# Performance work log

Measured on AMD Instinct MI355X. Metric: run time of the kernel, lower is better.

## Reference

```python
import jax, jax.numpy as jnp
import numpy as np

B, N, M = 16, 4096, 4096

def setup_inputs() -> dict:
    key = jax.random.key(0)
    k1, k2, k3 = jax.random.split(key, 3)
    src_points = jax.random.normal(k1, (B, N, 3), dtype=jnp.float32)
    tgt_points = jax.random.normal(k2, (B, M, 3), dtype=jnp.float32)
    weights = jax.random.uniform(k3, (B,), dtype=jnp.float32)
    return {"src_points": src_points, "tgt_points": tgt_points, "weights": weights}

def reference(src_points, tgt_points, weights):
    # Pairwise squared distances per batch: [B, N, M]
    # ||s - t||^2 = ||s||^2 + ||t||^2 - 2 s.t  (single dense intermediate)
    s2 = jnp.sum(src_points * src_points, axis=-1)  # [B, N]
    t2 = jnp.sum(tgt_points * tgt_points, axis=-1)  # [B, M]
    cross = jnp.einsum('bnd,bmd->bnm', src_points, tgt_points)  # [B, N, M]
    d2 = s2[:, :, None] + t2[:, None, :] - 2.0 * cross          # [B, N, M]
    d2 = jnp.maximum(d2, 0.0)  # numerical guard
    # Bidirectional chamfer: mean of nearest-neighbor squared distances
    d_src_to_tgt = jnp.mean(jnp.min(d2, axis=2), axis=1)  # [B]
    d_tgt_to_src = jnp.mean(jnp.min(d2, axis=1), axis=1)  # [B]
    distances = d_src_to_tgt + d_tgt_to_src               # [B]
    distances = distances * weights
    return jnp.mean(distances)  # reduction='mean'
```

## Files before the change

kernel.cpp:

```cpp
#include <hip/hip_runtime.h>

#define BQ 16
#define NP 4096
#define MP 4096

constexpr int TPB = 256;
constexpr int WAVES = 4;
constexpr int FR = 4;
constexpr int SRC_PER_BLOCK = 32 * FR * WAVES;
constexpr int TGT_PER_BLOCK = 1024;
constexpr int CHUNK = 256;

typedef __bf16 bf16x8 __attribute__((ext_vector_type(8)));
typedef float f32x16 __attribute__((ext_vector_type(16)));

union Frag {
    unsigned short u[8];
    bf16x8 v;
    int4 i4;
};

__device__ inline unsigned short f2bf(float f) {
    unsigned u = __float_as_uint(f);
    return (unsigned short)((u + 0x7FFFu + ((u >> 16) & 1u)) >> 16);
}
__device__ inline float bf2f(unsigned short h) {
    return __uint_as_float(((unsigned)h) << 16);
}

__global__ __launch_bounds__(TPB) void chamfer_prep_kernel(
    const float* __restrict__ srcp, const float* __restrict__ tgtp,
    unsigned short* __restrict__ table, unsigned int* __restrict__ minbuf,
    float* __restrict__ out) {
    const int idx = blockIdx.x * TPB + threadIdx.x;
    const int dir = idx >> 16;
    const int rem = idx & 65535;
    const float* rows = dir ? srcp : tgtp;
    const float* p = rows + (size_t)rem * 3;
    float x = p[0], y = p[1], z = p[2];
    unsigned short xh = f2bf(x), yh = f2bf(y), zh = f2bf(z);
    unsigned short xl = f2bf(x - bf2f(xh));
    unsigned short yl = f2bf(y - bf2f(yh));
    unsigned short zl = f2bf(z - bf2f(zh));
    float t2 = fmaf(x, x, fmaf(y, y, z * z));
    unsigned short t2h = f2bf(t2), t2l = f2bf(t2 - bf2f(t2h));
    const unsigned short ONE = 0x3F80;
    Frag p0, p1;
    p0.u[0] = xh; p0.u[1] = yh; p0.u[2] = zh;
    p0.u[3] = xh; p0.u[4] = yh; p0.u[5] = zh;
    p0.u[6] = xl; p0.u[7] = yl;
    p1.u[0] = zl;
    p1.u[1] = t2h; p1.u[2] = t2l;
    p1.u[3] = ONE; p1.u[4] = ONE;
    p1.u[5] = 0; p1.u[6] = 0; p1.u[7] = 0;
    int4* dst = (int4*)(table + (size_t)idx * 16);
    dst[0] = p0.i4;
    dst[1] = p1.i4;
    minbuf[idx] = 0x7F800000u;
    if (idx == 0) out[0] = 0.0f;
}

__global__ __launch_bounds__(TPB) void chamfer_main_kernel(
    const float* __restrict__ srcp, const float* __restrict__ tgtp,
    const unsigned short* __restrict__ table,
    unsigned int* __restrict__ minbuf) {
    const int gz  = blockIdx.z;
    const int dir = gz >> 4;
    const int b   = gz & 15;
    const float* S = dir ? (tgtp + (size_t)b * MP * 3) : (srcp + (size_t)b * NP * 3);
    const unsigned short* At =
        table + ((size_t)gz * 4096 + (size_t)blockIdx.y * TGT_PER_BLOCK) * 16;
    unsigned int* mb = minbuf + (size_t)gz * 4096;

    const int tid  = threadIdx.x;
    const int lane = tid & 63;
    const int half = lane >> 5;
    const int col  = lane & 31;
    const int wave = tid >> 6;

    __shared__ unsigned short sh[CHUNK * 16];
    const unsigned short ONE = 0x3F80;

    Frag bf[FR];
#pragma unroll
    for (int f = 0; f < FR; ++f) {
        const int sidx = blockIdx.x * SRC_PER_BLOCK + (wave * FR + f) * 32 + col;
        const float* sp = S + (size_t)sidx * 3;
        float x = sp[0], y = sp[1], z = sp[2];
        unsigned short uh0 = f2bf(-2.0f * x), uh1 = f2bf(-2.0f * y), uh2 = f2bf(-2.0f * z);
        unsigned short ul0 = f2bf(-2.0f * x - bf2f(uh0));
        unsigned short ul1 = f2bf(-2.0f * y - bf2f(uh1));
        unsigned short ul2 = f2bf(-2.0f * z - bf2f(uh2));
        float s2 = fmaf(x, x, fmaf(y, y, z * z));
        unsigned short s2h = f2bf(s2), s2l = f2bf(s2 - bf2f(s2h));
        if (half == 0) {
            bf[f].u[0] = uh0; bf[f].u[1] = uh1; bf[f].u[2] = uh2;
            bf[f].u[3] = ul0; bf[f].u[4] = ul1; bf[f].u[5] = ul2;
            bf[f].u[6] = uh0; bf[f].u[7] = uh1;
        } else {
            bf[f].u[0] = uh2; bf[f].u[1] = ONE; bf[f].u[2] = ONE;
            bf[f].u[3] = s2h; bf[f].u[4] = s2l;
            bf[f].u[5] = 0;   bf[f].u[6] = 0;  bf[f].u[7] = 0;
        }
    }

    float accm[FR];
#pragma unroll
    for (int f = 0; f < FR; ++f) accm[f] = __int_as_float(0x7F800000);

    const f32x16 zc = {};

    for (int c = 0; c < TGT_PER_BLOCK / CHUNK; ++c) {
        {
            const int4* gp = (const int4*)(At + (size_t)c * CHUNK * 16);
            int4* sp4 = (int4*)sh;
            sp4[tid]       = gp[tid];
            sp4[tid + 256] = gp[tid + 256];
        }
        __syncthreads();

#pragma unroll
        for (int sc = 0; sc < CHUNK / 32; ++sc) {
            Frag a;
            a.i4 = *(const int4*)&sh[sc * 512 + col * 16 + half * 8];
#pragma unroll
            for (int f = 0; f < FR; ++f) {
                f32x16 d = __builtin_amdgcn_mfma_f32_32x32x16_bf16(a.v, bf[f].v, zc, 0, 0, 0);
                float m0 = fminf(fminf(d[0], d[1]), d[2]);
                float m1 = fminf(fminf(d[3], d[4]), d[5]);
                float m2 = fminf(fminf(d[6], d[7]), d[8]);
                float m3 = fminf(fminf(d[9], d[10]), d[11]);
                float m4 = fminf(fminf(d[12], d[13]), d[14]);
                float t0 = fminf(fminf(m0, m1), m2);
                float t1 = fminf(fminf(m3, m4), d[15]);
                accm[f] = fminf(fminf(accm[f], t0), t1);
            }
        }
        __syncthreads();
    }

#pragma unroll
    for (int f = 0; f < FR; ++f) {
        float m = fminf(accm[f], __shfl_xor(accm[f], 32, 64));
        m = fmaxf(m, 0.0f);
        if (lane < 32) {
            const int sidx = blockIdx.x * SRC_PER_BLOCK + (wave * FR + f) * 32 + col;
            atomicMin(&mb[sidx], __float_as_uint(m));
        }
    }
}

__global__ __launch_bounds__(TPB) void chamfer_reduce_kernel(
    const float* __restrict__ minbuf, const float* __restrict__ weights,
    float* __restrict__ out) {
    const int idx = blockIdx.x;
    const int b = idx & 15;
    const float* m0 = minbuf + (size_t)idx * 4096;

    float s = 0.0f;
    for (int i = threadIdx.x; i < 4096; i += TPB) s += m0[i];
#pragma unroll
    for (int off = 32; off > 0; off >>= 1) s += __shfl_down(s, off, 64);

    __shared__ float red[TPB / 64];
    if ((threadIdx.x & 63) == 0) red[threadIdx.x >> 6] = s;
    __syncthreads();
    if (threadIdx.x == 0) {
        float tot = red[0] + red[1] + red[2] + red[3];
        atomicAdd(out, weights[b] * tot * (1.0f / (4096.0f * (float)BQ)));
    }
}

__global__ void chamfer_zero_kernel(float* __restrict__ out) { out[0] = 0.0f; }

__global__ __launch_bounds__(TPB) void chamfer_mfma_fb_kernel(
    const float* __restrict__ srcp, const float* __restrict__ tgtp,
    const float* __restrict__ wts, float* __restrict__ out) {
    const int gy = blockIdx.y, dir = gy >> 4, b = gy & 15;
    const float* S = dir ? (tgtp + (size_t)b * MP * 3) : (srcp + (size_t)b * NP * 3);
    const float* T = dir ? (srcp + (size_t)b * NP * 3) : (tgtp + (size_t)b * MP * 3);
    const int tid = threadIdx.x, lane = tid & 63, half = lane >> 5,
              col = tid & 31, wave = tid >> 6;
    __shared__ unsigned short sh[256 * 16];
    __shared__ float partial[4];
    const unsigned short ONE = 0x3F80;
    Frag bfrag;
    {
        const int sidx = blockIdx.x * 128 + wave * 32 + (lane & 31);
        const float* sp = S + (size_t)sidx * 3;
        float x = sp[0], y = sp[1], z = sp[2];
        unsigned short uh0 = f2bf(-2.0f * x), uh1 = f2bf(-2.0f * y), uh2 = f2bf(-2.0f * z);
        unsigned short ul0 = f2bf(-2.0f * x - bf2f(uh0));
        unsigned short ul1 = f2bf(-2.0f * y - bf2f(uh1));
        unsigned short ul2 = f2bf(-2.0f * z - bf2f(uh2));
        float s2 = fmaf(x, x, fmaf(y, y, z * z));
        unsigned short s2h = f2bf(s2), s2l = f2bf(s2 - bf2f(s2h));
        if (half == 0) {
            bfrag.u[0] = uh0; bfrag.u[1] = uh1; bfrag.u[2] = uh2;
            bfrag.u[3] = ul0; bfrag.u[4] = ul1; bfrag.u[5] = ul2;
            bfrag.u[6] = uh0; bfrag.u[7] = uh1;
        } else {
            bfrag.u[0] = uh2; bfrag.u[1] = ONE; bfrag.u[2] = ONE;
            bfrag.u[3] = s2h; bfrag.u[4] = s2l;
            bfrag.u[5] = 0;   bfrag.u[6] = 0;  bfrag.u[7] = 0;
        }
    }
    float accm = __int_as_float(0x7F800000);
    for (int c = 0; c < MP / 256; ++c) {
        {
            const float* tp = T + (size_t)(c * 256 + tid) * 3;
            float x = tp[0], y = tp[1], z = tp[2];
            unsigned short xh = f2bf(x), yh = f2bf(y), zh = f2bf(z);
            unsigned short xl = f2bf(x - bf2f(xh)), yl = f2bf(y - bf2f(yh)),
                           zl = f2bf(z - bf2f(zh));
            float t2 = fmaf(x, x, fmaf(y, y, z * z));
            unsigned short t2h = f2bf(t2), t2l = f2bf(t2 - bf2f(t2h));
            Frag p0, p1;
            p0.u[0] = xh; p0.u[1] = yh; p0.u[2] = zh;
            p0.u[3] = xh; p0.u[4] = yh; p0.u[5] = zh;
            p0.u[6] = xl; p0.u[7] = yl;
            p1.u[0] = zl; p1.u[1] = t2h; p1.u[2] = t2l;
            p1.u[3] = ONE; p1.u[4] = ONE; p1.u[5] = 0; p1.u[6] = 0; p1.u[7] = 0;
            const int sub = tid >> 5, row = tid & 31;
            *(int4*)&sh[sub * 512 + row * 8] = p0.i4;
            *(int4*)&sh[sub * 512 + 256 + row * 8] = p1.i4;
        }
        __syncthreads();
        const f32x16 zc = {};
#pragma unroll
        for (int sc = 0; sc < 8; ++sc) {
            Frag a;
            a.i4 = *(const int4*)&sh[sc * 512 + half * 256 + col * 8];
            f32x16 d = __builtin_amdgcn_mfma_f32_32x32x16_bf16(a.v, bfrag.v, zc, 0, 0, 0);
            float m0 = fminf(fminf(d[0], d[1]), d[2]);
            float m1 = fminf(fminf(d[3], d[4]), d[5]);
            float m2 = fminf(fminf(d[6], d[7]), d[8]);
            float m3 = fminf(fminf(d[9], d[10]), d[11]);
            float m4 = fminf(fminf(d[12], d[13]), d[14]);
            accm = fminf(accm, fminf(fminf(fminf(m0, m1), m2),
                                     fminf(fminf(m3, m4), d[15])));
        }
        __syncthreads();
    }
    float m = fminf(accm, __shfl_xor(accm, 32, 64));
    m = fmaxf(m, 0.0f);
#pragma unroll
    for (int off = 16; off > 0; off >>= 1) m += __shfl_xor(m, off, 64);
    if (lane == 0) partial[wave] = m;
    __syncthreads();
    if (tid == 0) {
        float v = partial[0] + partial[1] + partial[2] + partial[3];
        atomicAdd(out, v * wts[b] * (1.0f / ((float)NP * (float)BQ)));
    }
}

extern "C" void kernel_launch(void* const* d_in, const int* in_sizes, int n_in,
                              void* d_out, int out_size, void* d_ws, size_t ws_size,
                              hipStream_t stream) {
    const float* src = (const float*)d_in[0];
    const float* tgt = (const float*)d_in[1];
    const float* wts = (const float*)d_in[2];
    float* out = (float*)d_out;

    const size_t MINBUF_BYTES = (size_t)2 * BQ * 4096 * 4;
    const size_t TABLE_BYTES  = (size_t)2 * BQ * 4096 * 32;

    if (ws_size >= MINBUF_BYTES + TABLE_BYTES) {
        unsigned int* minbuf = (unsigned int*)d_ws;
        unsigned short* table = (unsigned short*)((char*)d_ws + MINBUF_BYTES);

        chamfer_prep_kernel<<<(2 * BQ * 4096) / TPB, TPB, 0, stream>>>(
            src, tgt, table, minbuf, out);

        dim3 grid(NP / SRC_PER_BLOCK, MP / TGT_PER_BLOCK, 2 * BQ);
        chamfer_main_kernel<<<grid, TPB, 0, stream>>>(src, tgt, table, minbuf);

        chamfer_reduce_kernel<<<2 * BQ, TPB, 0, stream>>>(
            (const float*)minbuf, wts, out);
    } else {
        chamfer_zero_kernel<<<1, 1, 0, stream>>>(out);
        dim3 grid(NP / 128, 2 * BQ);
        chamfer_mfma_fb_kernel<<<grid, TPB, 0, stream>>>(src, tgt, wts, out);
    }
}
```

Before: 93.37 us.

## Stream MFMA A-fragments directly from global table, dropping LDS staging and barriers

The main kernel no longer copies target chunks into shared memory with barriers. Each lane now loads its bf16 A-fragment straight from a prep-table layout reordered to match the MFMA fragment layout. The tiling also changes: two source fragments per wave instead of four and a target split of two, giving a different grid shape and fewer atomics per target. This removes LDS traffic and synchronisation but relies on global/L2 cache bandwidth, since four waves reread the same lines. The fallback kernel also gets a register-prefetch of the next chunk.

```diff
diff --git a/kernel.cpp b/kernel.cpp
--- a/kernel.cpp
+++ b/kernel.cpp
@@ -6,10 +6,10 @@
 
 constexpr int TPB = 256;
 constexpr int WAVES = 4;
-constexpr int FR = 4;
-constexpr int SRC_PER_BLOCK = 32 * FR * WAVES;
-constexpr int TGT_PER_BLOCK = 1024;
-constexpr int CHUNK = 256;
+constexpr int FR = 2;
+constexpr int COLS_PER_BLOCK = 32 * FR * WAVES;
+constexpr int ROWSPLIT = 2;
+constexpr int GROUPS_PER_BLOCK = (MP / 32) / ROWSPLIT;
 
 typedef __bf16 bf16x8 __attribute__((ext_vector_type(8)));
 typedef float f32x16 __attribute__((ext_vector_type(16)));
@@ -33,10 +33,12 @@
     unsigned short* __restrict__ table, unsigned int* __restrict__ minbuf,
     float* __restrict__ out) {
     const int idx = blockIdx.x * TPB + threadIdx.x;
-    const int dir = idx >> 16;
-    const int rem = idx & 65535;
-    const float* rows = dir ? srcp : tgtp;
-    const float* p = rows + (size_t)rem * 3;
+    const int gy  = idx >> 12;
+    const int t   = idx & 4095;
+    const int dir = gy >> 4, b = gy & 15;
+    const float* rows = dir ? (srcp + (size_t)b * NP * 3)
+                            : (tgtp + (size_t)b * MP * 3);
+    const float* p = rows + (size_t)t * 3;
     float x = p[0], y = p[1], z = p[2];
     unsigned short xh = f2bf(x), yh = f2bf(y), zh = f2bf(z);
     unsigned short xl = f2bf(x - bf2f(xh));
@@ -53,9 +55,9 @@
     p1.u[1] = t2h; p1.u[2] = t2l;
     p1.u[3] = ONE; p1.u[4] = ONE;
     p1.u[5] = 0; p1.u[6] = 0; p1.u[7] = 0;
-    int4* dst = (int4*)(table + (size_t)idx * 16);
-    dst[0] = p0.i4;
-    dst[1] = p1.i4;
+    unsigned short* dst = table + ((size_t)gy << 16) + ((t >> 5) << 9) + ((t & 31) << 4);
+    *(int4*)(dst)     = p0.i4;
+    *(int4*)(dst + 8) = p1.i4;
     minbuf[idx] = 0x7F800000u;
     if (idx == 0) out[0] = 0.0f;
 }
@@ -64,13 +66,11 @@
     const float* __restrict__ srcp, const float* __restrict__ tgtp,
     const unsigned short* __restrict__ table,
     unsigned int* __restrict__ minbuf) {
-    const int gz  = blockIdx.z;
-    const int dir = gz >> 4;
-    const int b   = gz & 15;
+    const int gy  = blockIdx.z;
+    const int dir = gy >> 4;
+    const int b   = gy & 15;
     const float* S = dir ? (tgtp + (size_t)b * MP * 3) : (srcp + (size_t)b * NP * 3);
-    const unsigned short* At =
-        table + ((size_t)gz * 4096 + (size_t)blockIdx.y * TGT_PER_BLOCK) * 16;
-    unsigned int* mb = minbuf + (size_t)gz * 4096;
+    unsigned int* mb = minbuf + ((size_t)gy << 12);
 
     const int tid  = threadIdx.x;
     const int lane = tid & 63;
@@ -78,13 +78,12 @@
     const int col  = lane & 31;
     const int wave = tid >> 6;
 
-    __shared__ unsigned short sh[CHUNK * 16];
     const unsigned short ONE = 0x3F80;
 
-    Frag bf[FR];
-#pragma unroll
-    for (int f = 0; f < FR; ++f) {
-        const int sidx = blockIdx.x * SRC_PER_BLOCK + (wave * FR + f) * 32 + col;
+    Frag bfr[FR];
+#pragma unroll
+    for (int f = 0; f < FR; ++f) {
+        const int sidx = blockIdx.x * COLS_PER_BLOCK + (wave * FR + f) * 32 + col;
         const float* sp = S + (size_t)sidx * 3;
         float x = sp[0], y = sp[1], z = sp[2];
         unsigned short uh0 = f2bf(-2.0f * x), uh1 = f2bf(-2.0f * y), uh2 = f2bf(-2.0f * z);
@@ -94,13 +93,13 @@
         float s2 = fmaf(x, x, fmaf(y, y, z * z));
         unsigned short s2h = f2bf(s2), s2l = f2bf(s2 - bf2f(s2h));
         if (half == 0) {
-            bf[f].u[0] = uh0; bf[f].u[1] = uh1; bf[f].u[2] = uh2;
-            bf[f].u[3] = ul0; bf[f].u[4] = ul1; bf[f].u[5] = ul2;
-            bf[f].u[6] = uh0; bf[f].u[7] = uh1;
+            bfr[f].u[0] = uh0; bfr[f].u[1] = uh1; bfr[f].u[2] = uh2;
+            bfr[f].u[3] = ul0; bfr[f].u[4] = ul1; bfr[f].u[5] = ul2;
+            bfr[f].u[6] = uh0; bfr[f].u[7] = uh1;
         } else {
-            bf[f].u[0] = uh2; bf[f].u[1] = ONE; bf[f].u[2] = ONE;
-            bf[f].u[3] = s2h; bf[f].u[4] = s2l;
-            bf[f].u[5] = 0;   bf[f].u[6] = 0;  bf[f].u[7] = 0;
+            bfr[f].u[0] = uh2; bfr[f].u[1] = ONE; bfr[f].u[2] = ONE;
+            bfr[f].u[3] = s2h; bfr[f].u[4] = s2l;
+            bfr[f].u[5] = 0;   bfr[f].u[6] = 0;  bfr[f].u[7] = 0;
         }
     }
 
@@ -110,33 +109,26 @@
 
     const f32x16 zc = {};
 
-    for (int c = 0; c < TGT_PER_BLOCK / CHUNK; ++c) {
-        {
-            const int4* gp = (const int4*)(At + (size_t)c * CHUNK * 16);
-            int4* sp4 = (int4*)sh;
-            sp4[tid]       = gp[tid];
-            sp4[tid + 256] = gp[tid + 256];
-        }
-        __syncthreads();
-
-#pragma unroll
-        for (int sc = 0; sc < CHUNK / 32; ++sc) {
-            Frag a;
-            a.i4 = *(const int4*)&sh[sc * 512 + col * 16 + half * 8];
-#pragma unroll
-            for (int f = 0; f < FR; ++f) {
-                f32x16 d = __builtin_amdgcn_mfma_f32_32x32x16_bf16(a.v, bf[f].v, zc, 0, 0, 0);
-                float m0 = fminf(fminf(d[0], d[1]), d[2]);
-                float m1 = fminf(fminf(d[3], d[4]), d[5]);
-                float m2 = fminf(fminf(d[6], d[7]), d[8]);
-                float m3 = fminf(fminf(d[9], d[10]), d[11]);
-                float m4 = fminf(fminf(d[12], d[13]), d[14]);
-                float t0 = fminf(fminf(m0, m1), m2);
-                float t1 = fminf(fminf(m3, m4), d[15]);
-                accm[f] = fminf(fminf(accm[f], t0), t1);
-            }
-        }
-        __syncthreads();
+    const unsigned short* lptr = table + ((size_t)gy << 16) +
+                                 ((size_t)blockIdx.y * GROUPS_PER_BLOCK << 9) +
+                                 (col << 4) + (half << 3);
+
+#pragma unroll 4
+    for (int g = 0; g < GROUPS_PER_BLOCK; ++g) {
+        Frag a;
+        a.i4 = *(const int4*)(lptr + ((size_t)g << 9));
+#pragma unroll
+        for (int f = 0; f < FR; ++f) {
+            f32x16 d = __builtin_amdgcn_mfma_f32_32x32x16_bf16(a.v, bfr[f].v, zc, 0, 0, 0);
+            float m0 = fminf(fminf(d[0], d[1]), d[2]);
+            float m1 = fminf(fminf(d[3], d[4]), d[5]);
+            float m2 = fminf(fminf(d[6], d[7]), d[8]);
+            float m3 = fminf(fminf(d[9], d[10]), d[11]);
+            float m4 = fminf(fminf(d[12], d[13]), d[14]);
+            float t0 = fminf(fminf(m0, m1), m2);
+            float t1 = fminf(fminf(m3, m4), d[15]);
+            accm[f] = fminf(fminf(accm[f], t0), t1);
+        }
     }
 
 #pragma unroll
@@ -144,7 +136,7 @@
         float m = fminf(accm[f], __shfl_xor(accm[f], 32, 64));
         m = fmaxf(m, 0.0f);
         if (lane < 32) {
-            const int sidx = blockIdx.x * SRC_PER_BLOCK + (wave * FR + f) * 32 + col;
+            const int sidx = blockIdx.x * COLS_PER_BLOCK + (wave * FR + f) * 32 + col;
             atomicMin(&mb[sidx], __float_as_uint(m));
         }
     }
@@ -155,7 +147,7 @@
     float* __restrict__ out) {
     const int idx = blockIdx.x;
     const int b = idx & 15;
-    const float* m0 = minbuf + (size_t)idx * 4096;
+    const float* m0 = minbuf + ((size_t)idx << 12);
 
     float s = 0.0f;
     for (int i = threadIdx.x; i < 4096; i += TPB) s += m0[i];
@@ -173,20 +165,21 @@
 
 __global__ void chamfer_zero_kernel(float* __restrict__ out) { out[0] = 0.0f; }
 
-__global__ __launch_bounds__(TPB) void chamfer_mfma_fb_kernel(
+__global__ __launch_bounds__(TPB) void chamfer_fb_kernel(
     const float* __restrict__ srcp, const float* __restrict__ tgtp,
     const float* __restrict__ wts, float* __restrict__ out) {
     const int gy = blockIdx.y, dir = gy >> 4, b = gy & 15;
     const float* S = dir ? (tgtp + (size_t)b * MP * 3) : (srcp + (size_t)b * NP * 3);
     const float* T = dir ? (srcp + (size_t)b * NP * 3) : (tgtp + (size_t)b * MP * 3);
     const int tid = threadIdx.x, lane = tid & 63, half = lane >> 5,
-              col = tid & 31, wave = tid >> 6;
+              col = lane & 31, wave = tid >> 6;
     __shared__ unsigned short sh[256 * 16];
-    __shared__ float partial[4];
+    __shared__ float partial[WAVES];
     const unsigned short ONE = 0x3F80;
-    Frag bfrag;
-    {
-        const int sidx = blockIdx.x * 128 + wave * 32 + (lane & 31);
+    Frag bfr[FR];
+#pragma unroll
+    for (int f = 0; f < FR; ++f) {
+        const int sidx = blockIdx.x * COLS_PER_BLOCK + (wave * FR + f) * 32 + col;
         const float* sp = S + (size_t)sidx * 3;
         float x = sp[0], y = sp[1], z = sp[2];
         unsigned short uh0 = f2bf(-2.0f * x), uh1 = f2bf(-2.0f * y), uh2 = f2bf(-2.0f * z);
@@ -196,24 +189,29 @@
         float s2 = fmaf(x, x, fmaf(y, y, z * z));
         unsigned short s2h = f2bf(s2), s2l = f2bf(s2 - bf2f(s2h));
         if (half == 0) {
-            bfrag.u[0] = uh0; bfrag.u[1] = uh1; bfrag.u[2] = uh2;
-            bfrag.u[3] = ul0; bfrag.u[4] = ul1; bfrag.u[5] = ul2;
-            bfrag.u[6] = uh0; bfrag.u[7] = uh1;
+            bfr[f].u[0] = uh0; bfr[f].u[1] = uh1; bfr[f].u[2] = uh2;
+            bfr[f].u[3] = ul0; bfr[f].u[4] = ul1; bfr[f].u[5] = ul2;
+            bfr[f].u[6] = uh0; bfr[f].u[7] = uh1;
         } else {
-            bfrag.u[0] = uh2; bfrag.u[1] = ONE; bfrag.u[2] = ONE;
-            bfrag.u[3] = s2h; bfrag.u[4] = s2l;
-            bfrag.u[5] = 0;   bfrag.u[6] = 0;  bfrag.u[7] = 0;
-        }
-    }
-    float accm = __int_as_float(0x7F800000);
+            bfr[f].u[0] = uh2; bfr[f].u[1] = ONE; bfr[f].u[2] = ONE;
+            bfr[f].u[3] = s2h; bfr[f].u[4] = s2l;
+            bfr[f].u[5] = 0;   bfr[f].u[6] = 0;  bfr[f].u[7] = 0;
+        }
+    }
+    float accm[FR];
+#pragma unroll
+    for (int f = 0; f < FR; ++f) accm[f] = __int_as_float(0x7F800000);
+    const f32x16 zc = {};
+    const int sub = tid >> 5, row = tid & 31;
+    float cx, cy, cz;
+    { const float* tp = T + (size_t)tid * 3; cx = tp[0]; cy = tp[1]; cz = tp[2]; }
     for (int c = 0; c < MP / 256; ++c) {
         {
-            const float* tp = T + (size_t)(c * 256 + tid) * 3;
-            float x = tp[0], y = tp[1], z = tp[2];
-            unsigned short xh = f2bf(x), yh = f2bf(y), zh = f2bf(z);
-            unsigned short xl = f2bf(x - bf2f(xh)), yl = f2bf(y - bf2f(yh)),
-                           zl = f2bf(z - bf2f(zh));
-            float t2 = fmaf(x, x, fmaf(y, y, z * z));
+            unsigned short xh = f2bf(cx), yh = f2bf(cy), zh = f2bf(cz);
+            unsigned short xl = f2bf(cx - bf2f(xh));
+            unsigned short yl = f2bf(cy - bf2f(yh));
+            unsigned short zl = f2bf(cz - bf2f(zh));
+            float t2 = fmaf(cx, cx, fmaf(cy, cy, cz * cz));
             unsigned short t2h = f2bf(t2), t2l = f2bf(t2 - bf2f(t2h));
             Frag p0, p1;
             p0.u[0] = xh; p0.u[1] = yh; p0.u[2] = zh;
@@ -221,32 +219,41 @@
             p0.u[6] = xl; p0.u[7] = yl;
             p1.u[0] = zl; p1.u[1] = t2h; p1.u[2] = t2l;
             p1.u[3] = ONE; p1.u[4] = ONE; p1.u[5] = 0; p1.u[6] = 0; p1.u[7] = 0;
-            const int sub = tid >> 5, row = tid & 31;
-            *(int4*)&sh[sub * 512 + row * 8] = p0.i4;
-            *(int4*)&sh[sub * 512 + 256 + row * 8] = p1.i4;
+            *(int4*)&sh[((sub * 2 + 0) * 32 + row) * 8] = p0.i4;
+            *(int4*)&sh[((sub * 2 + 1) * 32 + row) * 8] = p1.i4;
         }
         __syncthreads();
-        const f32x16 zc = {};
+        if (c + 1 < MP / 256) {
+            const float* tp = T + (size_t)((c + 1) * 256 + tid) * 3;
+            cx = tp[0]; cy = tp[1]; cz = tp[2];
+        }
 #pragma unroll
         for (int sc = 0; sc < 8; ++sc) {
             Frag a;
-            a.i4 = *(const int4*)&sh[sc * 512 + half * 256 + col * 8];
-            f32x16 d = __builtin_amdgcn_mfma_f32_32x32x16_bf16(a.v, bfrag.v, zc, 0, 0, 0);
-            float m0 = fminf(fminf(d[0], d[1]), d[2]);
-            float m1 = fminf(fminf(d[3], d[4]), d[5]);
-            float m2 = fminf(fminf(d[6], d[7]), d[8]);
-            float m3 = fminf(fminf(d[9], d[10]), d[11]);
-            float m4 = fminf(fminf(d[12], d[13]), d[14]);
-            accm = fminf(accm, fminf(fminf(fminf(m0, m1), m2),
-                                     fminf(fminf(m3, m4), d[15])));
+            a.i4 = *(const int4*)&sh[((sc * 2 + half) * 32 + col) * 8];
+#pragma unroll
+            for (int f = 0; f < FR; ++f) {
+                f32x16 d = __builtin_amdgcn_mfma_f32_32x32x16_bf16(a.v, bfr[f].v, zc, 0, 0, 0);
+                float m0 = fminf(fminf(d[0], d[1]), d[2]);
+                float m1 = fminf(fminf(d[3], d[4]), d[5]);
+                float m2 = fminf(fminf(d[6], d[7]), d[8]);
+                float m3 = fminf(fminf(d[9], d[10]), d[11]);
+                float m4 = fminf(fminf(d[12], d[13]), d[14]);
+                accm[f] = fminf(accm[f], fminf(fminf(fminf(m0, m1), m2),
+                                               fminf(fminf(m3, m4), d[15])));
+            }
         }
         __syncthreads();
     }
-    float m = fminf(accm, __shfl_xor(accm, 32, 64));
-    m = fmaxf(m, 0.0f);
-#pragma unroll
-    for (int off = 16; off > 0; off >>= 1) m += __shfl_xor(m, off, 64);
-    if (lane == 0) partial[wave] = m;
+    float tot = 0.0f;
+#pragma unroll
+    for (int f = 0; f < FR; ++f) {
+        float m = fminf(accm[f], __shfl_xor(accm[f], 32, 64));
+        tot += fmaxf(m, 0.0f);
+    }
+#pragma unroll
+    for (int off = 32; off > 0; off >>= 1) tot += __shfl_xor(tot, off, 64);
+    if (lane == 0) partial[wave] = tot * 0.5f;
     __syncthreads();
     if (tid == 0) {
         float v = partial[0] + partial[1] + partial[2] + partial[3];
@@ -266,20 +273,20 @@
     const size_t TABLE_BYTES  = (size_t)2 * BQ * 4096 * 32;
 
     if (ws_size >= MINBUF_BYTES + TABLE_BYTES) {
-        unsigned int* minbuf = (unsigned int*)d_ws;
+        unsigned int* minbuf  = (unsigned int*)d_ws;
         unsigned short* table = (unsigned short*)((char*)d_ws + MINBUF_BYTES);
 
         chamfer_prep_kernel<<<(2 * BQ * 4096) / TPB, TPB, 0, stream>>>(
             src, tgt, table, minbuf, out);
 
-        dim3 grid(NP / SRC_PER_BLOCK, MP / TGT_PER_BLOCK, 2 * BQ);
+        dim3 grid(NP / COLS_PER_BLOCK, ROWSPLIT, 2 * BQ);
         chamfer_main_kernel<<<grid, TPB, 0, stream>>>(src, tgt, table, minbuf);
 
         chamfer_reduce_kernel<<<2 * BQ, TPB, 0, stream>>>(
             (const float*)minbuf, wts, out);
     } else {
         chamfer_zero_kernel<<<1, 1, 0, stream>>>(out);
-        dim3 grid(NP / 128, 2 * BQ);
-        chamfer_mfma_fb_kernel<<<grid, TPB, 0, stream>>>(src, tgt, wts, out);
-    }
-}
+        dim3 grid(NP / COLS_PER_BLOCK, 2 * BQ);
+        chamfer_fb_kernel<<<grid, TPB, 0, stream>>>(src, tgt, wts, out);
+    }
+}
```

After: 99.36 us. 1.06x slower.
